# Optimization experiments

Measured on AMD Instinct MI355X. Metric: run time of the kernel, lower is better.

The kernel has to match this reference:

```python
import jax, jax.numpy as jnp
import numpy as np

B, OBS, H, D, E, T, A = 8192, 128, 512, 512, 16, 50, 32
LOG_STD_MIN, LOG_STD_MAX = -20.0, 2.0
ACT_LIMIT = 1.0


def setup_inputs() -> dict:
    key = jax.random.key(0)
    ks = jax.random.split(key, 24)
    s = 0.05  # weight init scale for MLP weights
    f32 = jnp.float32
    return {
        "obs": jax.random.normal(ks[0], (B, OBS), f32),
        "task": jax.random.randint(ks[1], (B,), 0, T),
        "eps": jax.random.normal(ks[2], (B, A), f32),
        # backbone: obs_dim -> 512 -> 512, relu after every layer
        "bW1": jax.random.normal(ks[3], (OBS, H), f32) * s, "bb1": jnp.zeros((H,), f32),
        "bW2": jax.random.normal(ks[4], (H, H), f32) * s, "bb2": jnp.zeros((H,), f32),
        # stacked expert MLPs: 512 -> 512(relu) -> 512(identity), batched over E
        "eW1": jax.random.normal(ks[5], (E, H, D), f32) * s, "eb1": jnp.zeros((E, D), f32),
        "eW2": jax.random.normal(ks[6], (E, D, D), f32) * s, "eb2": jnp.zeros((E, D), f32),
        # attention params (torch.randn init in original)
        "key_mats": jax.random.normal(ks[7], (E, D, D), f32),
        "value_mats": jax.random.normal(ks[8], (E, D, D), f32),
        "task_queries": jax.random.normal(ks[9], (T, D), f32),
        # mu tower: D -> 512(relu) -> act_dim
        "mW1": jax.random.normal(ks[10], (D, H), f32) * s, "mb1": jnp.zeros((H,), f32),
        "mW2": jax.random.normal(ks[11], (H, A), f32) * s, "mb2": jnp.zeros((A,), f32),
        # log_std tower: D -> 512(relu) -> act_dim
        "lW1": jax.random.normal(ks[12], (D, H), f32) * s, "lb1": jnp.zeros((H,), f32),
        "lW2": jax.random.normal(ks[13], (H, A), f32) * s, "lb2": jnp.zeros((A,), f32),
    }


def reference(obs, task, eps, bW1, bb1, bW2, bb2, eW1, eb1, eW2, eb2,
              key_mats, value_mats, task_queries,
              mW1, mb1, mW2, mb2, lW1, lb1, lW2, lb2):
    relu = jax.nn.relu
    # backbone (relu after both layers, incl. output_activation=activation)
    h = relu(obs @ bW1 + bb1)          # [B, H]
    h = relu(h @ bW2 + bb2)            # [B, H]
    # all experts as one batched GEMM (replaces jit.fork per-expert dispatch)
    eo = relu(jnp.einsum('bi,eij->bej', h, eW1) + eb1)   # [B, E, D]
    eo = jnp.einsum('bej,ejk->bek', eo, eW2) + eb2       # [B, E, D]
    # attention-weighted mixture of experts
    vals = jnp.einsum('bei,eij->bej', eo, value_mats)    # [B, E, D]
    keys = jnp.einsum('bei,eij->bej', eo, key_mats)      # [B, E, D]
    q = task_queries[task]                               # [B, D]
    w = jax.nn.softmax(jnp.einsum('bei,bi->be', keys, q), axis=-1)  # [B, E]
    tower = jnp.einsum('be,bei->bi', w, vals)            # [B, D]
    # squashed Gaussian head
    mu = relu(tower @ mW1 + mb1) @ mW2 + mb2             # [B, A]
    log_std = jnp.clip(relu(tower @ lW1 + lb1) @ lW2 + lb2, LOG_STD_MIN, LOG_STD_MAX)
    a = mu + jnp.exp(log_std) * eps                      # rsample with explicit noise
    # Normal log_prob of a = mu + std*eps, summed over action dim
    logp = jnp.sum(-0.5 * eps * eps - log_std - 0.5 * jnp.log(2.0 * jnp.pi), axis=-1)
    # tanh-squash correction
    logp = logp - jnp.sum(2.0 * (jnp.log(2.0) - a - jax.nn.softplus(-2.0 * a)), axis=-1)
    pi = ACT_LIMIT * jnp.tanh(a)
    return (pi, logp)
```

## Files before the change

### kernel.cpp

```cpp
#include <hip/hip_runtime.h>
#include <hip/hip_bf16.h>
#include <cstdint>


typedef _Float16 f16;
typedef _Float16 f16x4 __attribute__((ext_vector_type(4)));
typedef _Float16 f16x8 __attribute__((ext_vector_type(8)));
typedef float f32x4 __attribute__((ext_vector_type(4)));

__device__ __forceinline__ void fsplit(float x, f16& h, f16& l) {
    h = (f16)x;
    l = (f16)(x - (float)h);
}

__device__ __forceinline__ void gload16(const void* g, void* s) {
    __builtin_amdgcn_global_load_lds(
        (const __attribute__((address_space(1))) void*)g,
        (__attribute__((address_space(3))) void*)s, 16, 0, 0);
}

__global__ void split_pairs(const float* __restrict__ x, f16* __restrict__ h,
                            f16* __restrict__ l, int n4) {
    int i = blockIdx.x * 256 + threadIdx.x;
    if (i >= n4) return;
    float4 v = ((const float4*)x)[i];
    float a[4] = {v.x, v.y, v.z, v.w};
    f16x4 hh, ll;
#pragma unroll
    for (int j = 0; j < 4; ++j) { f16 hj, lj; fsplit(a[j], hj, lj); hh[j] = hj; ll[j] = lj; }
    *(f16x4*)&h[(long)i * 4] = hh;
    *(f16x4*)&l[(long)i * 4] = ll;
}

__global__ void transpose_split(const float* __restrict__ W, f16* __restrict__ Th,
                                f16* __restrict__ Tl, int K, int N, long ist, long ost) {
    __shared__ float t[32][33];
    const float* Wb = W + (long)blockIdx.z * ist;
    const int k0 = blockIdx.x * 32, n0 = blockIdx.y * 32;
    const int tid = threadIdx.x;
    const int r = tid >> 3, c4 = (tid & 7) * 4;
    float4 v = *(const float4*)&Wb[(long)(k0 + r) * N + n0 + c4];
    t[r][c4] = v.x; t[r][c4 + 1] = v.y; t[r][c4 + 2] = v.z; t[r][c4 + 3] = v.w;
    __syncthreads();
    f16x4 hh, ll;
#pragma unroll
    for (int j = 0; j < 4; ++j) { f16 hj, lj; fsplit(t[c4 + j][r], hj, lj); hh[j] = hj; ll[j] = lj; }
    long ob = (long)blockIdx.z * ost + (long)(n0 + r) * K + k0 + c4;
    *(f16x4*)&Th[ob] = hh;
    *(f16x4*)&Tl[ob] = ll;
}

__global__ void build_w2t(const float* __restrict__ mW2, const float* __restrict__ lW2,
                          float* __restrict__ W2T) {
    const int i = blockIdx.x * 256 + threadIdx.x;
    const int half = i >> 14, col = (i >> 9) & 31, k = i & 511;
    const float* src = half ? lW2 : mW2;
    W2T[i] = src[k * 32 + col];
}

__global__ void build_bcat(const float* __restrict__ mb1, const float* __restrict__ lb1,
                           float* __restrict__ bcat) {
    const int i = blockIdx.x * 256 + threadIdx.x;
    bcat[i] = (i < 512) ? mb1[i] : lb1[i - 512];
}

template <int OUTM, bool RELU, bool ASINGLE>
__global__ __launch_bounds__(256, ASINGLE ? 4 : 3) void gemm_pair(
    const f16* __restrict__ Ah, const f16* __restrict__ Al, int lda, long zsA,
    const f16* __restrict__ Bh, const f16* __restrict__ Bl, int ldb, long zsB,
    const float* __restrict__ bias, long zsBias,
    f16* __restrict__ Ch, f16* __restrict__ Cl, float* __restrict__ Cf,
    int ldc, long zsC, int K,
    const float* __restrict__ wscale,
    const int* __restrict__ task, const float* __restrict__ KQ2,
    float* __restrict__ scores) {
    __shared__ f16 As[ASINGLE ? 1 : 2][64][64];
    __shared__ f16 Bs[2][128][64];
    const int z = blockIdx.z;
    Ah += (long)z * zsA;
    if constexpr (!ASINGLE) Al += (long)z * zsA;
    Bh += (long)z * zsB; Bl += (long)z * zsB;
    if (bias) bias += (long)z * zsBias;
    if (OUTM <= 1) { Ch += (long)z * zsC; Cl += (long)z * zsC; }
    if (OUTM == 2 || OUTM == 3 || OUTM == 6) { Cf += (long)z * zsC; }
    const int tid = threadIdx.x;
    const int l = tid & 63;
    const int w = tid >> 6;
    const int row0 = blockIdx.x * 64;
    const int col0 = blockIdx.y * 128;
    const int wr = (w >> 1) * 32;
    const int wc = (w & 1) * 64;
    const int grow = l >> 3;
    const int gch = (l & 7) ^ grow;

    f32x4 acc[2][4];
#pragma unroll
    for (int mi = 0; mi < 2; ++mi)
#pragma unroll
        for (int ni = 0; ni < 4; ++ni)
#pragma unroll
            for (int j = 0; j < 4; ++j) acc[mi][ni][j] = 0.f;

    uint4 areg0, areg1; float ascl0, ascl1;
    auto ldA = [&](int k0) {
        const int r0 = w * 16 + grow, r1 = r0 + 8;
        const int scl = l & 7;
        areg0 = *(const uint4*)&Ah[(long)(row0 + r0) * lda + k0 + scl * 8];
        areg1 = *(const uint4*)&Ah[(long)(row0 + r1) * lda + k0 + scl * 8];
        const int e = k0 >> 9;
        ascl0 = wscale[(long)(row0 + r0) * 16 + e];
        ascl1 = wscale[(long)(row0 + r1) * 16 + e];
    };
    auto wrA = [&]() {
        const int scl = l & 7;
#pragma unroll
        for (int h = 0; h < 2; ++h) {
            const int r = w * 16 + grow + h * 8;
            const float s = h ? ascl1 : ascl0;
            f16x8 v = h ? *(f16x8*)&areg1 : *(f16x8*)&areg0;
#pragma unroll
            for (int j = 0; j < 8; ++j) v[j] = (f16)((float)v[j] * s);
            *(uint4*)&As[0][r][(scl ^ (r & 7)) * 8] = *(uint4*)&v;
        }
    };

    if constexpr (ASINGLE) ldA(0);
    for (int k0 = 0; k0 < K; k0 += 64) {
        __syncthreads();
        if constexpr (ASINGLE) {
            wrA();
            if (k0 + 64 < K) ldA(k0 + 64);
        } else {
            const long ga = (long)(row0 + w * 16 + grow) * lda + k0 + gch * 8;
            gload16(Ah + ga, &As[0][w * 16][0]);
            gload16(Ah + ga + (long)8 * lda, &As[0][w * 16 + 8][0]);
            gload16(Al + ga, &As[1][w * 16][0]);
            gload16(Al + ga + (long)8 * lda, &As[1][w * 16 + 8][0]);
        }
        {
            const long gb = (long)(col0 + w * 32 + grow) * ldb + k0 + gch * 8;
            gload16(Bh + gb, &Bs[0][w * 32][0]);
            gload16(Bh + gb + (long)8 * ldb, &Bs[0][w * 32 + 8][0]);
            gload16(Bh + gb + (long)16 * ldb, &Bs[0][w * 32 + 16][0]);
            gload16(Bh + gb + (long)24 * ldb, &Bs[0][w * 32 + 24][0]);
            gload16(Bl + gb, &Bs[1][w * 32][0]);
            gload16(Bl + gb + (long)8 * ldb, &Bs[1][w * 32 + 8][0]);
            gload16(Bl + gb + (long)16 * ldb, &Bs[1][w * 32 + 16][0]);
            gload16(Bl + gb + (long)24 * ldb, &Bs[1][w * 32 + 24][0]);
        }
        __syncthreads();
        const int r16 = l & 15, kg = l >> 4;
#pragma unroll
        for (int ks = 0; ks < 2; ++ks) {
            f16x8 a_h[2], a_l[2], b_h[4], b_l[4];
#pragma unroll
            for (int mi = 0; mi < 2; ++mi) {
                const int r = wr + mi * 16 + r16;
                const int off = ((ks * 4 + kg) ^ (r & 7)) * 8;
                a_h[mi] = *(const f16x8*)&As[0][r][off];
                if constexpr (!ASINGLE) a_l[mi] = *(const f16x8*)&As[1][r][off];
            }
#pragma unroll
            for (int ni = 0; ni < 4; ++ni) {
                const int c = wc + ni * 16 + r16;
                const int off = ((ks * 4 + kg) ^ (c & 7)) * 8;
                b_h[ni] = *(const f16x8*)&Bs[0][c][off];
                b_l[ni] = *(const f16x8*)&Bs[1][c][off];
            }
#pragma unroll
            for (int mi = 0; mi < 2; ++mi)
#pragma unroll
                for (int ni = 0; ni < 4; ++ni) {
                    acc[mi][ni] = __builtin_amdgcn_mfma_f32_16x16x32_f16(a_h[mi], b_h[ni], acc[mi][ni], 0, 0, 0);
                    acc[mi][ni] = __builtin_amdgcn_mfma_f32_16x16x32_f16(a_h[mi], b_l[ni], acc[mi][ni], 0, 0, 0);
                    if constexpr (!ASINGLE)
                        acc[mi][ni] = __builtin_amdgcn_mfma_f32_16x16x32_f16(a_l[mi], b_h[ni], acc[mi][ni], 0, 0, 0);
                }
        }
    }
    const int lane15 = l & 15;
    const int rsub = (l >> 4) * 4;
    if (OUTM == 5) {
        const int expert = col0 >> 9;
        float bv[4];
#pragma unroll
        for (int ni = 0; ni < 4; ++ni)
            bv[ni] = bias ? bias[col0 + wc + ni * 16 + lane15] : 0.f;
#pragma unroll
        for (int mi = 0; mi < 2; ++mi)
#pragma unroll
            for (int j = 0; j < 4; ++j) {
                const int rowg = row0 + wr + mi * 16 + rsub + j;
                const int t = task[rowg];
                const float* kqr = KQ2 + ((long)t * 16 + expert) * 512;
                float part = 0.f;
#pragma unroll
                for (int ni = 0; ni < 4; ++ni) {
                    const int colg = col0 + wc + ni * 16 + lane15;
                    float v = acc[mi][ni][j] + bv[ni];
                    if (RELU) v = fmaxf(v, 0.f);
                    Ch[(long)rowg * ldc + colg] = (f16)v;
                    part += v * kqr[colg & 511];
                }
#pragma unroll
                for (int d = 1; d < 16; d <<= 1) part += __shfl_xor(part, d);
                if (lane15 == 0) atomicAdd(&scores[rowg * 16 + expert], part);
            }
    } else {
#pragma unroll
        for (int mi = 0; mi < 2; ++mi)
#pragma unroll
            for (int ni = 0; ni < 4; ++ni) {
                const int colg = col0 + wc + ni * 16 + lane15;
                const float bv = bias ? bias[colg] : 0.f;
#pragma unroll
                for (int j = 0; j < 4; ++j) {
                    const int rowg = row0 + wr + mi * 16 + rsub + j;
                    float v = acc[mi][ni][j] + bv;
                    if (RELU) v = fmaxf(v, 0.f);
                    if (OUTM == 0) {
                        f16 hh, ll; fsplit(v, hh, ll);
                        const long idx = (long)rowg * ldc + colg;
                        Ch[idx] = hh; Cl[idx] = ll;
                    } else if (OUTM == 1) {
                        f16 hh, ll; fsplit(v, hh, ll);
                        const long idx = (long)colg * ldc + rowg;
                        Ch[idx] = hh; Cl[idx] = ll;
                    } else if (OUTM == 2) {
                        Cf[(long)rowg * ldc + colg] = v;
                    } else if (OUTM == 3) {
                        Cf[(long)rowg * ldc + colg] += v;
                    } else if (OUTM == 6) {
                        Cf[(long)colg * ldc + rowg] = v;
                    }
                }
            }
    }
}

__global__ void cb_from_kq(const f16* __restrict__ KqT_h, const f16* __restrict__ KqT_l,
                           const float* __restrict__ eb2, float* __restrict__ cb) {
    const int gw = (blockIdx.x * 256 + threadIdx.x) >> 6;
    const int l = threadIdx.x & 63;
    const int t = gw >> 4, e = gw & 15;
    const long base = (long)t * 8192 + e * 512 + l * 8;
    f16x8 hh = *(const f16x8*)&KqT_h[base];
    f16x8 ll = *(const f16x8*)&KqT_l[base];
    const float* bb = eb2 + e * 512 + l * 8;
    float s = 0.f;
#pragma unroll
    for (int j = 0; j < 8; ++j) s += ((float)hh[j] + (float)ll[j]) * bb[j];
#pragma unroll
    for (int d = 1; d < 64; d <<= 1) s += __shfl_xor(s, d);
    if (l == 0) cb[t * 16 + e] = s;
}

__global__ void bias_fold(const float* __restrict__ bvec, const float* __restrict__ M,
                          float* __restrict__ out) {
    const int gid = blockIdx.x * 256 + threadIdx.x;
    const int e = gid >> 9, j = gid & 511;
    const float* Me = M + (long)e * 262144;
    const float* be = bvec + e * 512;
    float s = 0.f;
    for (int k = 0; k < 512; ++k) s += be[k] * Me[(long)k * 512 + j];
    out[gid] = s;
}

__global__ void scores_init(const int* __restrict__ task, const float* __restrict__ cb,
                            float* __restrict__ sc) {
    const int i = blockIdx.x * 256 + threadIdx.x;
    sc[i] = cb[task[i >> 4] * 16 + (i & 15)];
}

__global__ void softmax16(float* __restrict__ sc) {
    const int b = blockIdx.x * 256 + threadIdx.x;
    float v[16];
    const float4* pp = (const float4*)&sc[b * 16];
#pragma unroll
    for (int qq = 0; qq < 4; ++qq) {
        float4 t = pp[qq];
        v[qq * 4] = t.x; v[qq * 4 + 1] = t.y; v[qq * 4 + 2] = t.z; v[qq * 4 + 3] = t.w;
    }
    float m = v[0];
#pragma unroll
    for (int e = 1; e < 16; ++e) m = fmaxf(m, v[e]);
    float ssum = 0.f;
#pragma unroll
    for (int e = 0; e < 16; ++e) { v[e] = expf(v[e] - m); ssum += v[e]; }
    const float inv = 1.f / ssum;
    float4* o = (float4*)&sc[b * 16];
#pragma unroll
    for (int qq = 0; qq < 4; ++qq) {
        float4 t;
        t.x = v[qq * 4] * inv; t.y = v[qq * 4 + 1] * inv;
        t.z = v[qq * 4 + 2] * inv; t.w = v[qq * 4 + 3] * inv;
        o[qq] = t;
    }
}

__global__ void wb_init(const float* __restrict__ w, const float* __restrict__ b2V,
                        float* __restrict__ towerAcc) {
    const int b = blockIdx.x;
    const int tid = threadIdx.x;
    float wv[16];
#pragma unroll
    for (int e = 0; e < 16; ++e) wv[e] = w[b * 16 + e];
#pragma unroll
    for (int rep = 0; rep < 2; ++rep) {
        const int j = rep * 256 + tid;
        float s = 0.f;
#pragma unroll
        for (int e = 0; e < 16; ++e) s += wv[e] * b2V[e * 512 + j];
        towerAcc[(long)b * 512 + j] = s;
    }
}

__global__ void head_kernel2(
    const f16* __restrict__ Rh, const f16* __restrict__ Rl,
    const float* __restrict__ W2T,
    const float* __restrict__ mb2, const float* __restrict__ lb2,
    const float* __restrict__ eps, float* __restrict__ pi, float* __restrict__ logp) {
    __shared__ float src[4][1032];
    const int tid = threadIdx.x, l = tid & 63, w = tid >> 6;
    const int b = blockIdx.x * 4 + w;
    const long rb = (long)b * 1024;
    {
        f16x8 h0 = *(const f16x8*)&Rh[rb + l * 8];
        f16x8 l0 = *(const f16x8*)&Rl[rb + l * 8];
        f16x8 h1 = *(const f16x8*)&Rh[rb + 512 + l * 8];
        f16x8 l1 = *(const f16x8*)&Rl[rb + 512 + l * 8];
#pragma unroll
        for (int j = 0; j < 8; ++j) {
            src[w][l * 8 + j] = (float)h0[j] + (float)l0[j];
            src[w][512 + l * 8 + j] = (float)h1[j] + (float)l1[j];
        }
    }
    __syncthreads();
    const int col = l & 31;
    const int half = l >> 5;
    const float4* wp = (const float4*)(W2T + ((long)(half * 32 + col)) * 512);
    const float4* sp = (const float4*)(&src[w][half * 512]);
    float a0 = 0.f, a1 = 0.f, a2 = 0.f, a3 = 0.f;
#pragma unroll 8
    for (int k4 = 0; k4 < 128; ++k4) {
        const float4 wv = wp[k4];
        const float4 sv = sp[k4];
        a0 = fmaf(wv.x, sv.x, a0);
        a1 = fmaf(wv.y, sv.y, a1);
        a2 = fmaf(wv.z, sv.z, a2);
        a3 = fmaf(wv.w, sv.w, a3);
    }
    const float* b2 = half ? lb2 : mb2;
    float s = b2[col] + ((a0 + a1) + (a2 + a3));
    const float other = __shfl_xor(s, 32);
    if (half == 0) {
        const float mu = s;
        float ls = fminf(fmaxf(other, -20.f), 2.f);
        const float e = eps[(long)b * 32 + col];
        const float a = mu + expf(ls) * e;
        float lt = -0.5f * e * e - ls - 0.91893853320467274f;
        const float x = -2.f * a;
        const float sp2 = fmaxf(x, 0.f) + log1pf(expf(-fabsf(x)));
        lt -= 2.f * (0.69314718055994531f - a - sp2);
        pi[(long)b * 32 + col] = tanhf(a);
        float r = lt;
#pragma unroll
        for (int d = 1; d < 32; d <<= 1) r += __shfl_xor(r, d);
        if (col == 0) logp[b] = r;
    }
}

extern "C" void kernel_launch(void* const* d_in, const int* in_sizes, int n_in,
                              void* d_out, int out_size, void* d_ws, size_t ws_size,
                              hipStream_t stream) {
    const float* obs = (const float*)d_in[0];
    const int* task = (const int*)d_in[1];
    const float* eps = (const float*)d_in[2];
    const float* bW1 = (const float*)d_in[3];
    const float* bb1 = (const float*)d_in[4];
    const float* bW2 = (const float*)d_in[5];
    const float* bb2 = (const float*)d_in[6];
    const float* eW1 = (const float*)d_in[7];
    const float* eb1 = (const float*)d_in[8];
    const float* eW2 = (const float*)d_in[9];
    const float* eb2 = (const float*)d_in[10];
    const float* keyM = (const float*)d_in[11];
    const float* valM = (const float*)d_in[12];
    const float* tq = (const float*)d_in[13];
    const float* mW1 = (const float*)d_in[14];
    const float* mb1 = (const float*)d_in[15];
    const float* mW2 = (const float*)d_in[16];
    const float* mb2 = (const float*)d_in[17];
    const float* lW1 = (const float*)d_in[18];
    const float* lb1 = (const float*)d_in[19];
    const float* lW2 = (const float*)d_in[20];
    const float* lb2 = (const float*)d_in[21];
    (void)in_sizes; (void)n_in; (void)out_size; (void)ws_size;

    const size_t MB = 1u << 20, KB = 1u << 10;
    char* base = (char*)d_ws;
    f16* eW1t_h = (f16*)(base + 0 * MB);   f16* eW1t_l = (f16*)(base + 8 * MB);
    f16* Wv2_h  = (f16*)(base + 16 * MB);  f16* Wv2_l  = (f16*)(base + 24 * MB);
    f16* eW2s_h = (f16*)(base + 32 * MB);  f16* eW2s_l = (f16*)(base + 40 * MB);
    f16* h2_h   = (f16*)(base + 32 * MB);  f16* h2_l   = (f16*)(base + 40 * MB);
    f16* t1_h   = (f16*)(base + 48 * MB);  f16* t1_l   = (f16*)(base + 56 * MB);
    f16* Rcat_l = (f16*)(base + 48 * MB);
    f16* Vt_h   = (f16*)(base + 64 * MB);  f16* Vt_l   = (f16*)(base + 72 * MB);
    f16* Rcat_h = (f16*)(base + 64 * MB);
    f16* keyMs_h = (f16*)(base + 80 * MB); f16* keyMs_l = (f16*)(base + 88 * MB);
    f16* KqT_h   = (f16*)(base + 96 * MB); f16* KqT_l   = (f16*)(base + 98 * MB);
    f16* tqP_h   = (f16*)(base + 100 * MB); f16* tqP_l  = (f16*)(base + 101 * MB);
    float* KQ2   = (float*)(base + 104 * MB);
    float* towerAcc = (float*)(base + 80 * MB);
    f16* twP_h  = (f16*)(base + 96 * MB);  f16* twP_l  = (f16*)(base + 104 * MB);
    f16* obs_h  = (f16*)(base + 112 * MB); f16* obs_l  = (f16*)(base + 114 * MB);
    char* q = base + 116 * MB;
    f16* bW1t_h = (f16*)q; q += 128 * KB;  f16* bW1t_l = (f16*)q; q += 128 * KB;
    f16* bW2t_h = (f16*)q; q += 512 * KB;  f16* bW2t_l = (f16*)q; q += 512 * KB;
    f16* mW1t_h = (f16*)q; q += 512 * KB;
    f16* lW1t_h = (f16*)q; q += 512 * KB;
    f16* mW1t_l = (f16*)q; q += 512 * KB;
    f16* lW1t_l = (f16*)q; q += 512 * KB;
    float* scores = (float*)q; q += 512 * KB;
    float* b2V    = (float*)q; q += 32 * KB;
    float* cb     = (float*)q; q += 16 * KB;
    float* W2T    = (float*)q; q += 128 * KB;
    float* bcat   = (float*)q; q += 16 * KB;
    f16* U = (f16*)(base + 122 * MB);

    const long EST = 262144;

    split_pairs<<<1024, 256, 0, stream>>>(obs, obs_h, obs_l, 262144);
    split_pairs<<<4096, 256, 0, stream>>>(eW2, eW2s_h, eW2s_l, 1048576);
    split_pairs<<<4096, 256, 0, stream>>>(keyM, keyMs_h, keyMs_l, 1048576);
    hipMemsetAsync(tqP_h, 0, 128 * 512 * sizeof(f16), stream);
    hipMemsetAsync(tqP_l, 0, 128 * 512 * sizeof(f16), stream);
    split_pairs<<<25, 256, 0, stream>>>(tq, tqP_h, tqP_l, 6400);
    transpose_split<<<dim3(4, 16, 1), 256, 0, stream>>>(bW1, bW1t_h, bW1t_l, 128, 512, 0, 0);
    transpose_split<<<dim3(16, 16, 1), 256, 0, stream>>>(bW2, bW2t_h, bW2t_l, 512, 512, 0, 0);
    transpose_split<<<dim3(16, 16, 1), 256, 0, stream>>>(mW1, mW1t_h, mW1t_l, 512, 512, 0, 0);
    transpose_split<<<dim3(16, 16, 1), 256, 0, stream>>>(lW1, lW1t_h, lW1t_l, 512, 512, 0, 0);
    transpose_split<<<dim3(16, 16, 16), 256, 0, stream>>>(eW1, eW1t_h, eW1t_l, 512, 512, EST, EST);
    transpose_split<<<dim3(16, 16, 16), 256, 0, stream>>>(valM, Vt_h, Vt_l, 512, 512, EST, EST);
    build_w2t<<<128, 256, 0, stream>>>(mW2, lW2, W2T);
    build_bcat<<<4, 256, 0, stream>>>(mb1, lb1, bcat);

    gemm_pair<1, false, false><<<dim3(8, 4, 16), 256, 0, stream>>>(
        eW2s_h, eW2s_l, 512, EST, Vt_h, Vt_l, 512, EST, nullptr, 0,
        Wv2_h, Wv2_l, nullptr, 8192, 512, 512, nullptr, nullptr, nullptr, nullptr);
    gemm_pair<1, false, false><<<dim3(128, 1, 1), 256, 0, stream>>>(
        keyMs_h, keyMs_l, 512, 0, tqP_h, tqP_l, 512, 0, nullptr, 0,
        KqT_h, KqT_l, nullptr, 8192, 0, 512, nullptr, nullptr, nullptr, nullptr);
    gemm_pair<6, false, false><<<dim3(8, 1, 16), 256, 0, stream>>>(
        eW2s_h, eW2s_l, 512, EST, KqT_h, KqT_l, 8192, 512, nullptr, 0,
        nullptr, nullptr, KQ2, 8192, 512, 512, nullptr, nullptr, nullptr, nullptr);
    cb_from_kq<<<200, 256, 0, stream>>>(KqT_h, KqT_l, eb2, cb);
    bias_fold<<<32, 256, 0, stream>>>(eb2, valM, b2V);

    gemm_pair<0, true, false><<<dim3(128, 4, 1), 256, 0, stream>>>(
        obs_h, obs_l, 128, 0, bW1t_h, bW1t_l, 128, 0, bb1, 0,
        t1_h, t1_l, nullptr, 512, 0, 128, nullptr, nullptr, nullptr, nullptr);
    gemm_pair<0, true, false><<<dim3(128, 4, 1), 256, 0, stream>>>(
        t1_h, t1_l, 512, 0, bW2t_h, bW2t_l, 512, 0, bb2, 0,
        h2_h, h2_l, nullptr, 512, 0, 512, nullptr, nullptr, nullptr, nullptr);

    scores_init<<<512, 256, 0, stream>>>(task, cb, scores);
    gemm_pair<5, true, false><<<dim3(128, 64, 1), 256, 0, stream>>>(
        h2_h, h2_l, 512, 0, eW1t_h, eW1t_l, 512, 0, eb1, 0,
        U, nullptr, nullptr, 8192, 0, 512, nullptr, task, KQ2, scores);
    softmax16<<<32, 256, 0, stream>>>(scores);

    wb_init<<<8192, 256, 0, stream>>>(scores, b2V, towerAcc);
    gemm_pair<3, false, true><<<dim3(128, 4, 1), 256, 0, stream>>>(
        U, nullptr, 8192, 0, Wv2_h, Wv2_l, 8192, 0, nullptr, 0,
        nullptr, nullptr, towerAcc, 512, 0, 8192, scores, nullptr, nullptr, nullptr);

    split_pairs<<<4096, 256, 0, stream>>>(towerAcc, twP_h, twP_l, 1048576);
    gemm_pair<0, true, false><<<dim3(128, 4, 2), 256, 0, stream>>>(
        twP_h, twP_l, 512, 0, mW1t_h, mW1t_l, 512, 262144, bcat, 512,
        Rcat_h, Rcat_l, nullptr, 1024, 512, 512, nullptr, nullptr, nullptr, nullptr);
    head_kernel2<<<2048, 256, 0, stream>>>(Rcat_h, Rcat_l, W2T, mb2, lb2, eps,
                                           (float*)d_out, (float*)d_out + 262144);
}
```

Measured before the change: 758.1 us.

## Drop low half of Wv2 split and fuse tower split into GEMM epilogue

```diff
diff --git a/kernel.cpp b/kernel.cpp
--- a/kernel.cpp
+++ b/kernel.cpp
@@ -64,7 +64,7 @@
     bcat[i] = (i < 512) ? mb1[i] : lb1[i - 512];
 }
 
-template <int OUTM, bool RELU, bool ASINGLE>
+template <int OUTM, bool RELU, bool ASINGLE, bool BSINGLE>
 __global__ __launch_bounds__(256, ASINGLE ? 4 : 3) void gemm_pair(
     const f16* __restrict__ Ah, const f16* __restrict__ Al, int lda, long zsA,
     const f16* __restrict__ Bh, const f16* __restrict__ Bl, int ldb, long zsB,
@@ -75,13 +75,15 @@
     const int* __restrict__ task, const float* __restrict__ KQ2,
     float* __restrict__ scores) {
     __shared__ f16 As[ASINGLE ? 1 : 2][64][64];
-    __shared__ f16 Bs[2][128][64];
+    __shared__ f16 Bs[BSINGLE ? 1 : 2][128][64];
     const int z = blockIdx.z;
     Ah += (long)z * zsA;
     if constexpr (!ASINGLE) Al += (long)z * zsA;
-    Bh += (long)z * zsB; Bl += (long)z * zsB;
+    Bh += (long)z * zsB;
+    if constexpr (!BSINGLE) Bl += (long)z * zsB;
     if (bias) bias += (long)z * zsBias;
     if (OUTM <= 1) { Ch += (long)z * zsC; Cl += (long)z * zsC; }
+    if (OUTM == 7) { Ch += (long)z * zsC; }
     if (OUTM == 2 || OUTM == 3 || OUTM == 6) { Cf += (long)z * zsC; }
     const int tid = threadIdx.x;
     const int l = tid & 63;
@@ -143,10 +145,12 @@
             gload16(Bh + gb + (long)8 * ldb, &Bs[0][w * 32 + 8][0]);
             gload16(Bh + gb + (long)16 * ldb, &Bs[0][w * 32 + 16][0]);
             gload16(Bh + gb + (long)24 * ldb, &Bs[0][w * 32 + 24][0]);
-            gload16(Bl + gb, &Bs[1][w * 32][0]);
-            gload16(Bl + gb + (long)8 * ldb, &Bs[1][w * 32 + 8][0]);
-            gload16(Bl + gb + (long)16 * ldb, &Bs[1][w * 32 + 16][0]);
-            gload16(Bl + gb + (long)24 * ldb, &Bs[1][w * 32 + 24][0]);
+            if constexpr (!BSINGLE) {
+                gload16(Bl + gb, &Bs[1][w * 32][0]);
+                gload16(Bl + gb + (long)8 * ldb, &Bs[1][w * 32 + 8][0]);
+                gload16(Bl + gb + (long)16 * ldb, &Bs[1][w * 32 + 16][0]);
+                gload16(Bl + gb + (long)24 * ldb, &Bs[1][w * 32 + 24][0]);
+            }
         }
         __syncthreads();
         const int r16 = l & 15, kg = l >> 4;
@@ -165,14 +169,15 @@
                 const int c = wc + ni * 16 + r16;
                 const int off = ((ks * 4 + kg) ^ (c & 7)) * 8;
                 b_h[ni] = *(const f16x8*)&Bs[0][c][off];
-                b_l[ni] = *(const f16x8*)&Bs[1][c][off];
+                if constexpr (!BSINGLE) b_l[ni] = *(const f16x8*)&Bs[1][c][off];
             }
 #pragma unroll
             for (int mi = 0; mi < 2; ++mi)
 #pragma unroll
                 for (int ni = 0; ni < 4; ++ni) {
                     acc[mi][ni] = __builtin_amdgcn_mfma_f32_16x16x32_f16(a_h[mi], b_h[ni], acc[mi][ni], 0, 0, 0);
-                    acc[mi][ni] = __builtin_amdgcn_mfma_f32_16x16x32_f16(a_h[mi], b_l[ni], acc[mi][ni], 0, 0, 0);
+                    if constexpr (!BSINGLE)
+                        acc[mi][ni] = __builtin_amdgcn_mfma_f32_16x16x32_f16(a_h[mi], b_l[ni], acc[mi][ni], 0, 0, 0);
                     if constexpr (!ASINGLE)
                         acc[mi][ni] = __builtin_amdgcn_mfma_f32_16x16x32_f16(a_l[mi], b_h[ni], acc[mi][ni], 0, 0, 0);
                 }
@@ -232,6 +237,13 @@
                         Cf[(long)rowg * ldc + colg] += v;
                     } else if (OUTM == 6) {
                         Cf[(long)colg * ldc + rowg] = v;
+                    } else if (OUTM == 7) {
+                        Ch[(long)colg * ldc + rowg] = (f16)v;
+                    } else if (OUTM == 8) {
+                        const long idx = (long)rowg * ldc + colg;
+                        v += Cf[idx];
+                        f16 hh, ll; fsplit(v, hh, ll);
+                        Ch[idx] = hh; Cl[idx] = ll;
                     }
                 }
             }
@@ -400,7 +412,7 @@
     const size_t MB = 1u << 20, KB = 1u << 10;
     char* base = (char*)d_ws;
     f16* eW1t_h = (f16*)(base + 0 * MB);   f16* eW1t_l = (f16*)(base + 8 * MB);
-    f16* Wv2_h  = (f16*)(base + 16 * MB);  f16* Wv2_l  = (f16*)(base + 24 * MB);
+    f16* Wv2_h  = (f16*)(base + 16 * MB);
     f16* eW2s_h = (f16*)(base + 32 * MB);  f16* eW2s_l = (f16*)(base + 40 * MB);
     f16* h2_h   = (f16*)(base + 32 * MB);  f16* h2_l   = (f16*)(base + 40 * MB);
     f16* t1_h   = (f16*)(base + 48 * MB);  f16* t1_l   = (f16*)(base + 56 * MB);
@@ -445,38 +457,37 @@
     build_w2t<<<128, 256, 0, stream>>>(mW2, lW2, W2T);
     build_bcat<<<4, 256, 0, stream>>>(mb1, lb1, bcat);
 
-    gemm_pair<1, false, false><<<dim3(8, 4, 16), 256, 0, stream>>>(
+    gemm_pair<7, false, false, false><<<dim3(8, 4, 16), 256, 0, stream>>>(
         eW2s_h, eW2s_l, 512, EST, Vt_h, Vt_l, 512, EST, nullptr, 0,
-        Wv2_h, Wv2_l, nullptr, 8192, 512, 512, nullptr, nullptr, nullptr, nullptr);
-    gemm_pair<1, false, false><<<dim3(128, 1, 1), 256, 0, stream>>>(
+        Wv2_h, nullptr, nullptr, 8192, 512, 512, nullptr, nullptr, nullptr, nullptr);
+    gemm_pair<1, false, false, false><<<dim3(128, 1, 1), 256, 0, stream>>>(
         keyMs_h, keyMs_l, 512, 0, tqP_h, tqP_l, 512, 0, nullptr, 0,
         KqT_h, KqT_l, nullptr, 8192, 0, 512, nullptr, nullptr, nullptr, nullptr);
-    gemm_pair<6, false, false><<<dim3(8, 1, 16), 256, 0, stream>>>(
+    gemm_pair<6, false, false, false><<<dim3(8, 1, 16), 256, 0, stream>>>(
         eW2s_h, eW2s_l, 512, EST, KqT_h, KqT_l, 8192, 512, nullptr, 0,
         nullptr, nullptr, KQ2, 8192, 512, 512, nullptr, nullptr, nullptr, nullptr);
     cb_from_kq<<<200, 256, 0, stream>>>(KqT_h, KqT_l, eb2, cb);
     bias_fold<<<32, 256, 0, stream>>>(eb2, valM, b2V);
 
-    gemm_pair<0, true, false><<<dim3(128, 4, 1), 256, 0, stream>>>(
+    gemm_pair<0, true, false, false><<<dim3(128, 4, 1), 256, 0, stream>>>(
         obs_h, obs_l, 128, 0, bW1t_h, bW1t_l, 128, 0, bb1, 0,
         t1_h, t1_l, nullptr, 512, 0, 128, nullptr, nullptr, nullptr, nullptr);
-    gemm_pair<0, true, false><<<dim3(128, 4, 1), 256, 0, stream>>>(
+    gemm_pair<0, true, false, false><<<dim3(128, 4, 1), 256, 0, stream>>>(
         t1_h, t1_l, 512, 0, bW2t_h, bW2t_l, 512, 0, bb2, 0,
         h2_h, h2_l, nullptr, 512, 0, 512, nullptr, nullptr, nullptr, nullptr);
 
     scores_init<<<512, 256, 0, stream>>>(task, cb, scores);
-    gemm_pair<5, true, false><<<dim3(128, 64, 1), 256, 0, stream>>>(
+    gemm_pair<5, true, false, false><<<dim3(128, 64, 1), 256, 0, stream>>>(
         h2_h, h2_l, 512, 0, eW1t_h, eW1t_l, 512, 0, eb1, 0,
         U, nullptr, nullptr, 8192, 0, 512, nullptr, task, KQ2, scores);
     softmax16<<<32, 256, 0, stream>>>(scores);
 
     wb_init<<<8192, 256, 0, stream>>>(scores, b2V, towerAcc);
-    gemm_pair<3, false, true><<<dim3(128, 4, 1), 256, 0, stream>>>(
-        U, nullptr, 8192, 0, Wv2_h, Wv2_l, 8192, 0, nullptr, 0,
-        nullptr, nullptr, towerAcc, 512, 0, 8192, scores, nullptr, nullptr, nullptr);
-
-    split_pairs<<<4096, 256, 0, stream>>>(towerAcc, twP_h, twP_l, 1048576);
-    gemm_pair<0, true, false><<<dim3(128, 4, 2), 256, 0, stream>>>(
+    gemm_pair<8, false, true, true><<<dim3(128, 4, 1), 256, 0, stream>>>(
+        U, nullptr, 8192, 0, Wv2_h, nullptr, 8192, 0, nullptr, 0,
+        twP_h, twP_l, towerAcc, 512, 0, 8192, scores, nullptr, nullptr, nullptr);
+
+    gemm_pair<0, true, false, false><<<dim3(128, 4, 2), 256, 0, stream>>>(
         twP_h, twP_l, 512, 0, mW1t_h, mW1t_l, 512, 262144, bcat, 512,
         Rcat_h, Rcat_l, nullptr, 1024, 512, 512, nullptr, nullptr, nullptr, nullptr);
     head_kernel2<<<2048, 256, 0, stream>>>(Rcat_h, Rcat_l, W2T, mb2, lb2, eps,
```

Result: faster. 705.4 us (-7.0%).
